# Kernel tuning notes

Hardware: AMD Instinct MI355X
Metric: run time of the kernel (lower is better)

Reference implementation:

```python
import jax, jax.numpy as jnp
import numpy as np

B, N, E, D, H, L = 1024, 64, 1024, 128, 4, 2
C = D // H          # per-head out_channels
K = 5               # options per attribute
LN_EPS = 1e-5


def setup_inputs() -> dict:
    key = jax.random.key(0)
    ks = jax.random.split(key, 22)
    s = 0.05
    inp = {
        'x': jax.random.randint(ks[0], (B, N), 0, K),
        'edge_index': jax.random.randint(ks[1], (2, E), 0, N),
        'edge_attr': jax.random.uniform(ks[2], (E, 1), jnp.float32),
        # tokenizer params
        'attr_emb': jax.random.normal(ks[3], (N, D), jnp.float32) * s,
        'opt_emb': jax.random.normal(ks[4], (N, K, D), jnp.float32) * s,
        'prior': jnp.ones((N, 1), jnp.float32),
        # GATv2 params, stacked over layers
        'Wl': jax.random.normal(ks[5], (L, D, D), jnp.float32) * s,
        'bl': jnp.zeros((L, D), jnp.float32),
        'Wr': jax.random.normal(ks[6], (L, D, D), jnp.float32) * s,
        'br': jnp.zeros((L, D), jnp.float32),
        'We': jax.random.normal(ks[7], (L, 1, D), jnp.float32) * s,
        'att': jax.random.normal(ks[8], (L, H, C), jnp.float32) * s,
        'conv_bias': jnp.zeros((L, D), jnp.float32),
        'ln_g': jnp.ones((L, D), jnp.float32),
        'ln_b': jnp.zeros((L, D), jnp.float32),
        # reliability head
        'W1': jax.random.normal(ks[9], (2 * D, D), jnp.float32) * s,
        'b1': jnp.zeros((D,), jnp.float32),
        'W2': jax.random.normal(ks[10], (D, 1), jnp.float32) * s,
        'b2': jnp.zeros((1,), jnp.float32),
    }
    return inp


def _forward(x, edge_index, edge_attr, attr_emb, opt_emb, prior,
             Wl, bl, Wr, br, We, att, conv_bias, ln_g, ln_b, W1, b1, W2, b2):
    Bb, n = x.shape
    # Tokenizer: token_i = p_i * (E_attr[i] + E_val[i](x_i))
    val = opt_emb[jnp.arange(n)[None, :], x]                 # [B,n,D]
    T0 = (attr_emb[None] + val) * prior[None]                # [B,n,D]

    src, dst = edge_index[0], edge_index[1]
    h = T0
    for l in range(Wl.shape[0]):
        xl = (h @ Wl[l] + bl[l]).reshape(Bb, n, H, C)        # source transform
        xr = (h @ Wr[l] + br[l]).reshape(Bb, n, H, C)        # target transform
        e = (edge_attr @ We[l]).reshape(1, E, H, C)          # edge embedding
        msg = xl[:, src]                                     # [B,E,H,C]
        z = jax.nn.leaky_relu(msg + xr[:, dst] + e, 0.2)
        alpha = jnp.einsum('behc,hc->beh', z, att[l])        # [B,E,H]
        # segment softmax over incoming edges per target node
        mx = jnp.full((Bb, n, H), -jnp.inf, alpha.dtype).at[:, dst].max(alpha)
        ex = jnp.exp(alpha - mx[:, dst])
        den = jnp.zeros((Bb, n, H), alpha.dtype).at[:, dst].add(ex)
        a = ex / den[:, dst]                                 # normalized attention
        out = jnp.zeros((Bb, n, H, C), h.dtype).at[:, dst].add(msg * a[..., None])
        g = out.reshape(Bb, n, D) + conv_bias[l]
        mu = g.mean(-1, keepdims=True)
        var = g.var(-1, keepdims=True)
        g = (g - mu) / jnp.sqrt(var + LN_EPS) * ln_g[l] + ln_b[l]
        g = jax.nn.elu(g)
        h = h + g                                            # residual

    hat_T = jnp.concatenate([T0, h], axis=-1)                # [B,n,2D]
    rel = jax.nn.sigmoid(jax.nn.relu(hat_T @ W1 + b1) @ W2 + b2)[..., 0]  # [B,n]
    rw = rel[..., None]
    f_scale = (h * rw).sum(1) / (rw.sum(1) + 1e-8)           # [B,D]
    return f_scale, rel, hat_T


def reference(x, edge_index, edge_attr, attr_emb, opt_emb, prior,
              Wl, bl, Wr, br, We, att, conv_bias, ln_g, ln_b, W1, b1, W2, b2):
    return _forward(x, edge_index, edge_attr, attr_emb, opt_emb, prior,
                    Wl, bl, Wr, br, We, att, conv_bias, ln_g, ln_b, W1, b1, W2, b2)
```

## Files before the change

kernel.cpp:

```cpp
#include <hip/hip_runtime.h>
#include <hip/hip_bf16.h>

#define Bv 1024
#define Nv 64
#define Ev 1024
#define Dv 128
#define Hv 4
#define Lv 2
#define Kv 5
#define PAD 130

typedef __hip_bfloat16 bf16;
typedef __attribute__((ext_vector_type(8))) short bf16x8_t;
typedef __attribute__((ext_vector_type(4))) float f32x4_t;

__device__ __forceinline__ float b2f(bf16 v) { return __bfloat162float(v); }
__device__ __forceinline__ bf16  f2b(float v) { return __float2bfloat16(v); }

__device__ bf16 g_pWl[(size_t)Lv * 2 * Dv * Dv];
__device__ bf16 g_pWr[(size_t)Lv * 2 * Dv * Dv];
__device__ bf16 g_pW1[(size_t)2 * 2 * Dv * Dv];

__device__ __forceinline__ void unpack2(unsigned int u, float& lo, float& hi) {
    union { unsigned int u; float f; } a, b;
    a.u = u << 16;
    b.u = u & 0xffff0000u;
    lo = a.f; hi = b.f;
}

__device__ __forceinline__ bf16x8_t load_a_frag(const bf16* buf, int elem_idx) {
    const unsigned int* p = (const unsigned int*)buf;
    union { bf16x8_t v; unsigned int u[4]; } r;
    int d = elem_idx >> 1;
    r.u[0] = p[d]; r.u[1] = p[d + 1]; r.u[2] = p[d + 2]; r.u[3] = p[d + 3];
    return r.v;
}

__global__ void build_csr(const int* __restrict__ edge_index,
                          int* __restrict__ off, int* __restrict__ eid)
{
    __shared__ int cnt[Nv];
    int tid = threadIdx.x;
    if (tid < Nv) cnt[tid] = 0;
    __syncthreads();
    for (int e = tid; e < Ev; e += blockDim.x)
        atomicAdd(&cnt[edge_index[Ev + e]], 1);
    __syncthreads();
    if (tid == 0) {
        int s = 0;
        for (int t = 0; t < Nv; ++t) { int c = cnt[t]; off[t] = s; cnt[t] = s; s += c; }
        off[Nv] = s;
    }
    __syncthreads();
    for (int e = tid; e < Ev; e += blockDim.x) {
        int d = edge_index[Ev + e];
        int pos = atomicAdd(&cnt[d], 1);
        eid[pos] = e;
    }
}

__device__ void pack_mat(const float* __restrict__ W, bf16* __restrict__ out,
                         int K, int tid, int nth)
{
    const int total = K * 128;
    for (int e = tid; e < total; e += nth) {
        int f    = e >> 9;
        int rem  = e & 511;
        int lane = rem >> 3;
        int i    = rem & 7;
        int kk   = f >> 3;
        int nt   = f & 7;
        int col  = nt * 16 + (lane & 15);
        int k    = kk * 32 + (lane >> 4) * 8 + i;
        float w  = W[k * 128 + col];
        bf16 hi  = f2b(w);
        out[e]         = hi;
        out[total + e] = f2b(w - b2f(hi));
    }
}

__global__ void pack_weights(const float* __restrict__ Wl, const float* __restrict__ Wr,
                             const float* __restrict__ W1)
{
    const int nth = gridDim.x * blockDim.x;
    const int tid = blockIdx.x * blockDim.x + threadIdx.x;
    for (int l = 0; l < Lv; ++l) {
        pack_mat(Wl + (size_t)l * Dv * Dv, g_pWl + (size_t)l * 2 * Dv * Dv, Dv, tid, nth);
        pack_mat(Wr + (size_t)l * Dv * Dv, g_pWr + (size_t)l * 2 * Dv * Dv, Dv, tid, nth);
    }
    pack_mat(W1, g_pW1, 2 * Dv, tid, nth);
}

__global__ __launch_bounds__(512, 2)
void gat_fused(const int* __restrict__ x, const int* __restrict__ edge_index,
               const float* __restrict__ edge_attr, const float* __restrict__ attr_emb,
               const float* __restrict__ opt_emb, const float* __restrict__ prior,
               const float* __restrict__ bl, const float* __restrict__ br,
               const float* __restrict__ We, const float* __restrict__ att,
               const float* __restrict__ conv_bias, const float* __restrict__ ln_g,
               const float* __restrict__ ln_b,
               const float* __restrict__ b1, const float* __restrict__ W2,
               const float* __restrict__ b2,
               const int* __restrict__ csr_off, const int* __restrict__ csr_eid,
               float* __restrict__ out_fscale, float* __restrict__ out_rel,
               float* __restrict__ out_hatT)
{
    const int b = blockIdx.x;
    const int tid = threadIdx.x;

    __shared__ __align__(16) bf16 hs [Nv * PAD];
    __shared__ __align__(16) bf16 xls[Nv * PAD];
    __shared__ __align__(16) bf16 xrs[Nv * PAD];
    __shared__ bf16 alphas[Ev * Hv];
    __shared__ float red [Nv * 8];
    __shared__ float red2[Nv * 8];
    __shared__ float wecol[Dv];
    __shared__ float attv [Dv];
    __shared__ float relbuf[Nv];

    for (int idx = tid; idx < Nv * Dv; idx += 512) {
        int n = idx >> 7, d = idx & 127;
        float t0 = (attr_emb[n * Dv + d] + opt_emb[(n * Kv + x[b * Nv + n]) * Dv + d])
                   * prior[n];
        hs[n * PAD + d] = f2b(t0);
    }

    for (int l = 0; l < Lv; ++l) {
        if (tid < Dv) {
            wecol[tid] = We[l * Dv + tid];
            attv[tid]  = att[l * Dv + tid];
        }
        __syncthreads();

        {
            const int w = tid >> 6, lane = tid & 63;
            const int row16 = lane & 15, kg = lane >> 4;
            const bf16* pB = (w < 4) ? (g_pWl + (size_t)l * 2 * Dv * Dv)
                                     : (g_pWr + (size_t)l * 2 * Dv * Dv);
            const int wc = (w & 3) * 32;
            f32x4_t acc[4][2];
            #pragma unroll
            for (int mt = 0; mt < 4; ++mt)
                #pragma unroll
                for (int nt = 0; nt < 2; ++nt)
                    acc[mt][nt] = (f32x4_t){0.f, 0.f, 0.f, 0.f};

            #pragma unroll
            for (int kk = 0; kk < 4; ++kk) {
                const int kb = kk * 32 + kg * 8;
                bf16x8_t a[4];
                #pragma unroll
                for (int mt = 0; mt < 4; ++mt)
                    a[mt] = load_a_frag(hs, (mt * 16 + row16) * PAD + kb);
                #pragma unroll
                for (int nt = 0; nt < 2; ++nt) {
                    const int f = kk * 8 + (w & 3) * 2 + nt;
                    bf16x8_t bh  = *(const bf16x8_t*)&pB[(size_t)(f * 64 + lane) * 8];
                    bf16x8_t blo = *(const bf16x8_t*)&pB[Dv * Dv + (size_t)(f * 64 + lane) * 8];
                    #pragma unroll
                    for (int mt = 0; mt < 4; ++mt) {
                        acc[mt][nt] = __builtin_amdgcn_mfma_f32_16x16x32_bf16(
                                          a[mt], bh, acc[mt][nt], 0, 0, 0);
                        acc[mt][nt] = __builtin_amdgcn_mfma_f32_16x16x32_bf16(
                                          a[mt], blo, acc[mt][nt], 0, 0, 0);
                    }
                }
            }
            bf16* dst = (w < 4) ? xls : xrs;
            const float* bias = (w < 4) ? (bl + l * Dv) : (br + l * Dv);
            #pragma unroll
            for (int mt = 0; mt < 4; ++mt)
                #pragma unroll
                for (int nt = 0; nt < 2; ++nt) {
                    const int col = wc + nt * 16 + row16;
                    #pragma unroll
                    for (int r = 0; r < 4; ++r) {
                        const int row = mt * 16 + kg * 4 + r;
                        dst[row * PAD + col] = f2b(acc[mt][nt][r] + bias[col]);
                    }
                }
        }
        __syncthreads();

        {
            const int h = (tid >> 6) & 3, half = tid >> 8, lane = tid & 63;
            for (int it = 0; it < 8; ++it) {
                int e = (half * 8 + it) * 64 + lane;
                int s = edge_index[e], t = edge_index[Ev + e];
                float ea = edge_attr[e];
                float acc = 0.f;
                int bs = s * PAD + h * 32, bt = t * PAD + h * 32;
                #pragma unroll
                for (int c = 0; c < 32; c += 2) {
                    float xl0, xl1, xr0, xr1;
                    unpack2(*(const unsigned int*)&xls[bs + c], xl0, xl1);
                    unpack2(*(const unsigned int*)&xrs[bt + c], xr0, xr1);
                    float z0 = xl0 + xr0 + ea * wecol[h * 32 + c];
                    float z1 = xl1 + xr1 + ea * wecol[h * 32 + c + 1];
                    z0 = z0 > 0.f ? z0 : 0.2f * z0;
                    z1 = z1 > 0.f ? z1 : 0.2f * z1;
                    acc += z0 * attv[h * 32 + c] + z1 * attv[h * 32 + c + 1];
                }
                alphas[e * Hv + h] = f2b(acc);
            }
        }
        __syncthreads();

        {
            const int t = tid & 63, h = (tid >> 6) & 3, half = tid >> 8;
            const int ch0 = h * 32 + half * 16;
            int beg = csr_off[t], end = csr_off[t + 1];
            float mx = -3e38f;
            for (int idx = beg; idx < end; ++idx)
                mx = fmaxf(mx, b2f(alphas[csr_eid[idx] * Hv + h]));
            float acc[16];
            #pragma unroll
            for (int c = 0; c < 16; ++c) acc[c] = 0.f;
            float den = 0.f;
            for (int idx = beg; idx < end; ++idx) {
                int e = csr_eid[idx];
                int s = edge_index[e];
                float ex = expf(b2f(alphas[e * Hv + h]) - mx);
                den += ex;
                int bs = s * PAD + ch0;
                #pragma unroll
                for (int c = 0; c < 16; c += 2) {
                    float m0, m1;
                    unpack2(*(const unsigned int*)&xls[bs + c], m0, m1);
                    acc[c] += ex * m0; acc[c + 1] += ex * m1;
                }
            }
            float inv_den = (end > beg) ? 1.f / den : 0.f;
            float sum = 0.f, sumsq = 0.f;
            #pragma unroll
            for (int c = 0; c < 16; ++c) {
                float g = acc[c] * inv_den + conv_bias[l * Dv + ch0 + c];
                acc[c] = g;
                sum += g; sumsq += g * g;
            }
            red [t * 8 + h * 2 + half] = sum;
            red2[t * 8 + h * 2 + half] = sumsq;
            __syncthreads();
            float mu = 0.f, ms = 0.f;
            #pragma unroll
            for (int j = 0; j < 8; ++j) { mu += red[t * 8 + j]; ms += red2[t * 8 + j]; }
            mu *= (1.f / 128.f); ms *= (1.f / 128.f);
            float rstd = rsqrtf(ms - mu * mu + 1e-5f);
            #pragma unroll
            for (int c = 0; c < 16; ++c) {
                float g = (acc[c] - mu) * rstd * ln_g[l * Dv + ch0 + c]
                          + ln_b[l * Dv + ch0 + c];
                g = g > 0.f ? g : (expf(g) - 1.f);
                int hi = t * PAD + ch0 + c;
                hs[hi] = f2b(b2f(hs[hi]) + g);
            }
        }
        __syncthreads();
    }

    if (tid < Dv) wecol[tid] = W2[tid];
    for (int idx = tid; idx < Nv * Dv; idx += 512) {
        int n = idx >> 7, d = idx & 127;
        float t0 = (attr_emb[n * Dv + d] + opt_emb[(n * Kv + x[b * Nv + n]) * Dv + d])
                   * prior[n];
        xrs[n * PAD + d] = f2b(t0);
        size_t rb = ((size_t)(b * Nv + n)) * (2 * Dv);
        out_hatT[rb + d]      = t0;
        out_hatT[rb + Dv + d] = b2f(hs[n * PAD + d]);
    }
    __syncthreads();

    {
        const int w = tid >> 6, lane = tid & 63;
        const int row16 = lane & 15, kg = lane >> 4;
        f32x4_t acc[4];
        #pragma unroll
        for (int mt = 0; mt < 4; ++mt)
            acc[mt] = (f32x4_t){0.f, 0.f, 0.f, 0.f};

        #pragma unroll
        for (int kk = 0; kk < 8; ++kk) {
            const bf16* asrc = (kk < 4) ? xrs : hs;
            const int kb = (kk & 3) * 32 + kg * 8;
            bf16x8_t a[4];
            #pragma unroll
            for (int mt = 0; mt < 4; ++mt)
                a[mt] = load_a_frag(asrc, (mt * 16 + row16) * PAD + kb);
            const int f = kk * 8 + w;
            bf16x8_t bh  = *(const bf16x8_t*)&g_pW1[(size_t)(f * 64 + lane) * 8];
            bf16x8_t blo = *(const bf16x8_t*)&g_pW1[(size_t)2 * Dv * Dv + (size_t)(f * 64 + lane) * 8];
            #pragma unroll
            for (int mt = 0; mt < 4; ++mt) {
                acc[mt] = __builtin_amdgcn_mfma_f32_16x16x32_bf16(a[mt], bh,  acc[mt], 0, 0, 0);
                acc[mt] = __builtin_amdgcn_mfma_f32_16x16x32_bf16(a[mt], blo, acc[mt], 0, 0, 0);
            }
        }
        #pragma unroll
        for (int mt = 0; mt < 4; ++mt) {
            const int col = w * 16 + row16;
            #pragma unroll
            for (int r = 0; r < 4; ++r) {
                const int row = mt * 16 + kg * 4 + r;
                float v = acc[mt][r] + b1[col];
                xls[row * PAD + col] = f2b(v > 0.f ? v : 0.f);
            }
        }
    }
    __syncthreads();

    {
        const int t = tid & 63, h = (tid >> 6) & 3, half = tid >> 8;
        const int ch0 = h * 32 + half * 16;
        float s = 0.f;
        #pragma unroll
        for (int c = 0; c < 16; c += 2) {
            float h0, h1;
            unpack2(*(const unsigned int*)&xls[t * PAD + ch0 + c], h0, h1);
            s += h0 * wecol[ch0 + c] + h1 * wecol[ch0 + c + 1];
        }
        red[t * 8 + h * 2 + half] = s;
        __syncthreads();
        if (h == 0 && half == 0) {
            float z = b2[0];
            #pragma unroll
            for (int j = 0; j < 8; ++j) z += red[t * 8 + j];
            float r = 1.f / (1.f + expf(-z));
            relbuf[t] = r;
            out_rel[b * Nv + t] = r;
        }
    }
    __syncthreads();

    if (tid < Dv) {
        float num = 0.f, den = 0.f;
        for (int n = 0; n < Nv; ++n) {
            float r = relbuf[n];
            num += b2f(hs[n * PAD + tid]) * r;
            den += r;
        }
        out_fscale[b * Dv + tid] = num / (den + 1e-8f);
    }
}

extern "C" void kernel_launch(void* const* d_in, const int* in_sizes, int n_in,
                              void* d_out, int out_size, void* d_ws, size_t ws_size,
                              hipStream_t stream)
{
    const int*   x          = (const int*)  d_in[0];
    const int*   edge_index = (const int*)  d_in[1];
    const float* edge_attr  = (const float*)d_in[2];
    const float* attr_emb   = (const float*)d_in[3];
    const float* opt_emb    = (const float*)d_in[4];
    const float* prior      = (const float*)d_in[5];
    const float* Wl         = (const float*)d_in[6];
    const float* bl         = (const float*)d_in[7];
    const float* Wr         = (const float*)d_in[8];
    const float* br         = (const float*)d_in[9];
    const float* We         = (const float*)d_in[10];
    const float* att        = (const float*)d_in[11];
    const float* conv_bias  = (const float*)d_in[12];
    const float* ln_g       = (const float*)d_in[13];
    const float* ln_b       = (const float*)d_in[14];
    const float* W1         = (const float*)d_in[15];
    const float* b1         = (const float*)d_in[16];
    const float* W2         = (const float*)d_in[17];
    const float* b2         = (const float*)d_in[18];

    int* csr_off = (int*)d_ws;
    int* csr_eid = (int*)d_ws + 128;

    float* out        = (float*)d_out;
    float* out_fscale = out;
    float* out_rel    = out + (size_t)Bv * Dv;
    float* out_hatT   = out + (size_t)Bv * Dv + (size_t)Bv * Nv;

    build_csr<<<1, 256, 0, stream>>>(edge_index, csr_off, csr_eid);
    pack_weights<<<64, 256, 0, stream>>>(Wl, Wr, W1);
    gat_fused<<<Bv, 512, 0, stream>>>(x, edge_index, edge_attr, attr_emb, opt_emb,
                                      prior, bl, br, We, att, conv_bias,
                                      ln_g, ln_b, b1, W2, b2,
                                      csr_off, csr_eid,
                                      out_fscale, out_rel, out_hatT);
}
```

Measured before the change: 309.6 us.

## Rewrite LeakyReLU attention as linear terms plus ReLU, pack f32x2 math, merge prep kernels

Uses the identity leaky(z) = 0.2*z + 0.8*relu(z) so the linear part of the attention score factors into per-node dot products (att·xl, att·xr), computed once per node, plus a per-head constant for the edge term. The per-edge loop keeps only a max with zero and packed two-wide FMAs. The aggregation, LayerNorm and reliability-head loops are rewritten with f32x2 vector types to encourage packed FP32 instructions. The CSR build and weight-packing kernels are merged into one launch, which also precomputes the edge constant. This adds an extra reduction pass and barrier per layer and changes rounding, since the per-node dot products come from bf16 values.

```diff
diff --git a/kernel.cpp b/kernel.cpp
--- a/kernel.cpp
+++ b/kernel.cpp
@@ -13,6 +13,7 @@
 typedef __hip_bfloat16 bf16;
 typedef __attribute__((ext_vector_type(8))) short bf16x8_t;
 typedef __attribute__((ext_vector_type(4))) float f32x4_t;
+typedef __attribute__((ext_vector_type(2))) float f32x2_t;
 
 __device__ __forceinline__ float b2f(bf16 v) { return __bfloat162float(v); }
 __device__ __forceinline__ bf16  f2b(float v) { return __float2bfloat16(v); }
@@ -20,12 +21,26 @@
 __device__ bf16 g_pWl[(size_t)Lv * 2 * Dv * Dv];
 __device__ bf16 g_pWr[(size_t)Lv * 2 * Dv * Dv];
 __device__ bf16 g_pW1[(size_t)2 * 2 * Dv * Dv];
+__device__ float g_K[Lv * Hv];
 
 __device__ __forceinline__ void unpack2(unsigned int u, float& lo, float& hi) {
     union { unsigned int u; float f; } a, b;
     a.u = u << 16;
     b.u = u & 0xffff0000u;
     lo = a.f; hi = b.f;
+}
+
+__device__ __forceinline__ f32x2_t unpack2v(unsigned int u) {
+    union { unsigned int u; float f; } a, b;
+    a.u = u << 16;
+    b.u = u & 0xffff0000u;
+    return (f32x2_t){a.f, b.f};
+}
+
+__device__ __forceinline__ unsigned int pack2v(f32x2_t v) {
+    union { bf16 b; unsigned short u; } lo, hi;
+    lo.b = f2b(v.x); hi.b = f2b(v.y);
+    return (unsigned int)lo.u | ((unsigned int)hi.u << 16);
 }
 
 __device__ __forceinline__ bf16x8_t load_a_frag(const bf16* buf, int elem_idx) {
@@ -34,29 +49,6 @@
     int d = elem_idx >> 1;
     r.u[0] = p[d]; r.u[1] = p[d + 1]; r.u[2] = p[d + 2]; r.u[3] = p[d + 3];
     return r.v;
-}
-
-__global__ void build_csr(const int* __restrict__ edge_index,
-                          int* __restrict__ off, int* __restrict__ eid)
-{
-    __shared__ int cnt[Nv];
-    int tid = threadIdx.x;
-    if (tid < Nv) cnt[tid] = 0;
-    __syncthreads();
-    for (int e = tid; e < Ev; e += blockDim.x)
-        atomicAdd(&cnt[edge_index[Ev + e]], 1);
-    __syncthreads();
-    if (tid == 0) {
-        int s = 0;
-        for (int t = 0; t < Nv; ++t) { int c = cnt[t]; off[t] = s; cnt[t] = s; s += c; }
-        off[Nv] = s;
-    }
-    __syncthreads();
-    for (int e = tid; e < Ev; e += blockDim.x) {
-        int d = edge_index[Ev + e];
-        int pos = atomicAdd(&cnt[d], 1);
-        eid[pos] = e;
-    }
 }
 
 __device__ void pack_mat(const float* __restrict__ W, bf16* __restrict__ out,
@@ -79,16 +71,48 @@
     }
 }
 
-__global__ void pack_weights(const float* __restrict__ Wl, const float* __restrict__ Wr,
-                             const float* __restrict__ W1)
+__global__ void prep(const int* __restrict__ edge_index,
+                     int* __restrict__ off, int* __restrict__ eid,
+                     const float* __restrict__ Wl, const float* __restrict__ Wr,
+                     const float* __restrict__ W1, const float* __restrict__ We,
+                     const float* __restrict__ att)
 {
-    const int nth = gridDim.x * blockDim.x;
-    const int tid = blockIdx.x * blockDim.x + threadIdx.x;
+    const int bid = blockIdx.x;
+    if (bid == 0) {
+        __shared__ int cnt[Nv];
+        int tid = threadIdx.x;
+        if (tid < Nv) cnt[tid] = 0;
+        __syncthreads();
+        for (int e = tid; e < Ev; e += blockDim.x)
+            atomicAdd(&cnt[edge_index[Ev + e]], 1);
+        __syncthreads();
+        if (tid == 0) {
+            int s = 0;
+            for (int t = 0; t < Nv; ++t) { int c = cnt[t]; off[t] = s; cnt[t] = s; s += c; }
+            off[Nv] = s;
+        }
+        __syncthreads();
+        for (int e = tid; e < Ev; e += blockDim.x) {
+            int d = edge_index[Ev + e];
+            int pos = atomicAdd(&cnt[d], 1);
+            eid[pos] = e;
+        }
+        return;
+    }
+    const int nth = 64 * 256;
+    const int tid = (bid - 1) * 256 + threadIdx.x;
     for (int l = 0; l < Lv; ++l) {
         pack_mat(Wl + (size_t)l * Dv * Dv, g_pWl + (size_t)l * 2 * Dv * Dv, Dv, tid, nth);
         pack_mat(Wr + (size_t)l * Dv * Dv, g_pWr + (size_t)l * 2 * Dv * Dv, Dv, tid, nth);
     }
     pack_mat(W1, g_pW1, 2 * Dv, tid, nth);
+    if (bid == 1 && threadIdx.x < Lv * Hv) {
+        int l = threadIdx.x / Hv, h = threadIdx.x % Hv;
+        float k = 0.f;
+        for (int c = 0; c < 32; ++c)
+            k += att[l * Dv + h * 32 + c] * We[l * Dv + h * 32 + c];
+        g_K[threadIdx.x] = 0.2f * k;
+    }
 }
 
 __global__ __launch_bounds__(512, 2)
@@ -96,11 +120,11 @@
                const float* __restrict__ edge_attr, const float* __restrict__ attr_emb,
                const float* __restrict__ opt_emb, const float* __restrict__ prior,
                const float* __restrict__ bl, const float* __restrict__ br,
-               const float* __restrict__ We, const float* __restrict__ att,
                const float* __restrict__ conv_bias, const float* __restrict__ ln_g,
                const float* __restrict__ ln_b,
                const float* __restrict__ b1, const float* __restrict__ W2,
                const float* __restrict__ b2,
+               const float* __restrict__ We, const float* __restrict__ att,
                const int* __restrict__ csr_off, const int* __restrict__ csr_eid,
                float* __restrict__ out_fscale, float* __restrict__ out_rel,
                float* __restrict__ out_hatT)
@@ -112,10 +136,10 @@
     __shared__ __align__(16) bf16 xls[Nv * PAD];
     __shared__ __align__(16) bf16 xrs[Nv * PAD];
     __shared__ bf16 alphas[Ev * Hv];
-    __shared__ float red [Nv * 8];
-    __shared__ float red2[Nv * 8];
-    __shared__ float wecol[Dv];
-    __shared__ float attv [Dv];
+    __shared__ __align__(16) float red [Nv * 8];
+    __shared__ __align__(16) float red2[Nv * 8];
+    __shared__ __align__(16) float wecol[Dv];
+    __shared__ __align__(16) float attv [Dv];
     __shared__ float relbuf[Nv];
 
     for (int idx = tid; idx < Nv * Dv; idx += 512) {
@@ -183,25 +207,44 @@
         __syncthreads();
 
         {
+            const int t = tid & 63, h = (tid >> 6) & 3, half = tid >> 8;
+            const int ch0 = h * 32 + half * 16;
+            f32x2_t dl2 = {0.f, 0.f}, dr2 = {0.f, 0.f};
+            #pragma unroll
+            for (int c = 0; c < 16; c += 2) {
+                f32x2_t a2 = *(const f32x2_t*)&attv[ch0 + c];
+                dl2 += a2 * unpack2v(*(const unsigned int*)&xls[t * PAD + ch0 + c]);
+                dr2 += a2 * unpack2v(*(const unsigned int*)&xrs[t * PAD + ch0 + c]);
+            }
+            red [t * 8 + h * 2 + half] = dl2.x + dl2.y;
+            red2[t * 8 + h * 2 + half] = dr2.x + dr2.y;
+        }
+        __syncthreads();
+
+        {
             const int h = (tid >> 6) & 3, half = tid >> 8, lane = tid & 63;
+            const float k02 = g_K[l * Hv + h];
+            const f32x2_t zero2 = {0.f, 0.f};
             for (int it = 0; it < 8; ++it) {
                 int e = (half * 8 + it) * 64 + lane;
                 int s = edge_index[e], t = edge_index[Ev + e];
                 float ea = edge_attr[e];
-                float acc = 0.f;
+                f32x2_t ea2 = {ea, ea};
+                f32x2_t acc2 = {0.f, 0.f};
                 int bs = s * PAD + h * 32, bt = t * PAD + h * 32;
                 #pragma unroll
                 for (int c = 0; c < 32; c += 2) {
-                    float xl0, xl1, xr0, xr1;
-                    unpack2(*(const unsigned int*)&xls[bs + c], xl0, xl1);
-                    unpack2(*(const unsigned int*)&xrs[bt + c], xr0, xr1);
-                    float z0 = xl0 + xr0 + ea * wecol[h * 32 + c];
-                    float z1 = xl1 + xr1 + ea * wecol[h * 32 + c + 1];
-                    z0 = z0 > 0.f ? z0 : 0.2f * z0;
-                    z1 = z1 > 0.f ? z1 : 0.2f * z1;
-                    acc += z0 * attv[h * 32 + c] + z1 * attv[h * 32 + c + 1];
+                    f32x2_t xl2 = unpack2v(*(const unsigned int*)&xls[bs + c]);
+                    f32x2_t xr2 = unpack2v(*(const unsigned int*)&xrs[bt + c]);
+                    f32x2_t we2 = *(const f32x2_t*)&wecol[h * 32 + c];
+                    f32x2_t at2 = *(const f32x2_t*)&attv [h * 32 + c];
+                    f32x2_t v   = xl2 + xr2 + ea2 * we2;
+                    acc2 += at2 * __builtin_elementwise_max(v, zero2);
                 }
-                alphas[e * Hv + h] = f2b(acc);
+                float dL = red [s * 8 + h * 2] + red [s * 8 + h * 2 + 1];
+                float dR = red2[t * 8 + h * 2] + red2[t * 8 + h * 2 + 1];
+                float alpha = 0.2f * (dL + dR) + k02 * ea + 0.8f * (acc2.x + acc2.y);
+                alphas[e * Hv + h] = f2b(alpha);
             }
         }
         __syncthreads();
@@ -213,46 +256,50 @@
             float mx = -3e38f;
             for (int idx = beg; idx < end; ++idx)
                 mx = fmaxf(mx, b2f(alphas[csr_eid[idx] * Hv + h]));
-            float acc[16];
-            #pragma unroll
-            for (int c = 0; c < 16; ++c) acc[c] = 0.f;
+            f32x2_t acc2[8];
+            #pragma unroll
+            for (int j = 0; j < 8; ++j) acc2[j] = (f32x2_t){0.f, 0.f};
             float den = 0.f;
             for (int idx = beg; idx < end; ++idx) {
                 int e = csr_eid[idx];
                 int s = edge_index[e];
                 float ex = expf(b2f(alphas[e * Hv + h]) - mx);
                 den += ex;
+                f32x2_t ex2 = {ex, ex};
                 int bs = s * PAD + ch0;
                 #pragma unroll
-                for (int c = 0; c < 16; c += 2) {
-                    float m0, m1;
-                    unpack2(*(const unsigned int*)&xls[bs + c], m0, m1);
-                    acc[c] += ex * m0; acc[c + 1] += ex * m1;
-                }
+                for (int j = 0; j < 8; ++j)
+                    acc2[j] += ex2 * unpack2v(*(const unsigned int*)&xls[bs + 2 * j]);
             }
             float inv_den = (end > beg) ? 1.f / den : 0.f;
-            float sum = 0.f, sumsq = 0.f;
-            #pragma unroll
-            for (int c = 0; c < 16; ++c) {
-                float g = acc[c] * inv_den + conv_bias[l * Dv + ch0 + c];
-                acc[c] = g;
-                sum += g; sumsq += g * g;
-            }
-            red [t * 8 + h * 2 + half] = sum;
-            red2[t * 8 + h * 2 + half] = sumsq;
+            f32x2_t id2 = {inv_den, inv_den};
+            f32x2_t sum2 = {0.f, 0.f}, sq2 = {0.f, 0.f};
+            #pragma unroll
+            for (int j = 0; j < 8; ++j) {
+                f32x2_t cb = *(const f32x2_t*)&conv_bias[l * Dv + ch0 + 2 * j];
+                f32x2_t g  = acc2[j] * id2 + cb;
+                acc2[j] = g;
+                sum2 += g; sq2 += g * g;
+            }
+            red [t * 8 + h * 2 + half] = sum2.x + sum2.y;
+            red2[t * 8 + h * 2 + half] = sq2.x + sq2.y;
             __syncthreads();
             float mu = 0.f, ms = 0.f;
             #pragma unroll
             for (int j = 0; j < 8; ++j) { mu += red[t * 8 + j]; ms += red2[t * 8 + j]; }
             mu *= (1.f / 128.f); ms *= (1.f / 128.f);
             float rstd = rsqrtf(ms - mu * mu + 1e-5f);
-            #pragma unroll
-            for (int c = 0; c < 16; ++c) {
-                float g = (acc[c] - mu) * rstd * ln_g[l * Dv + ch0 + c]
-                          + ln_b[l * Dv + ch0 + c];
-                g = g > 0.f ? g : (expf(g) - 1.f);
-                int hi = t * PAD + ch0 + c;
-                hs[hi] = f2b(b2f(hs[hi]) + g);
+            f32x2_t mu2 = {mu, mu}, rs2 = {rstd, rstd};
+            #pragma unroll
+            for (int j = 0; j < 8; ++j) {
+                f32x2_t lg = *(const f32x2_t*)&ln_g[l * Dv + ch0 + 2 * j];
+                f32x2_t lb = *(const f32x2_t*)&ln_b[l * Dv + ch0 + 2 * j];
+                f32x2_t g  = (acc2[j] - mu2) * rs2 * lg + lb;
+                g.x = g.x > 0.f ? g.x : (expf(g.x) - 1.f);
+                g.y = g.y > 0.f ? g.y : (expf(g.y) - 1.f);
+                unsigned int* hp = (unsigned int*)&hs[t * PAD + ch0 + 2 * j];
+                f32x2_t hv = unpack2v(*hp) + g;
+                *hp = pack2v(hv);
             }
         }
         __syncthreads();
@@ -311,14 +358,13 @@
     {
         const int t = tid & 63, h = (tid >> 6) & 3, half = tid >> 8;
         const int ch0 = h * 32 + half * 16;
-        float s = 0.f;
+        f32x2_t s2 = {0.f, 0.f};
         #pragma unroll
         for (int c = 0; c < 16; c += 2) {
-            float h0, h1;
-            unpack2(*(const unsigned int*)&xls[t * PAD + ch0 + c], h0, h1);
-            s += h0 * wecol[ch0 + c] + h1 * wecol[ch0 + c + 1];
-        }
-        red[t * 8 + h * 2 + half] = s;
+            f32x2_t h2 = unpack2v(*(const unsigned int*)&xls[t * PAD + ch0 + c]);
+            s2 += h2 * *(const f32x2_t*)&wecol[ch0 + c];
+        }
+        red[t * 8 + h * 2 + half] = s2.x + s2.y;
         __syncthreads();
         if (h == 0 && half == 0) {
             float z = b2[0];
@@ -374,11 +420,10 @@
     float* out_rel    = out + (size_t)Bv * Dv;
     float* out_hatT   = out + (size_t)Bv * Dv + (size_t)Bv * Nv;
 
-    build_csr<<<1, 256, 0, stream>>>(edge_index, csr_off, csr_eid);
-    pack_weights<<<64, 256, 0, stream>>>(Wl, Wr, W1);
+    prep<<<65, 256, 0, stream>>>(edge_index, csr_off, csr_eid, Wl, Wr, W1, We, att);
     gat_fused<<<Bv, 512, 0, stream>>>(x, edge_index, edge_attr, attr_emb, opt_emb,
-                                      prior, bl, br, We, att, conv_bias,
-                                      ln_g, ln_b, b1, W2, b2,
+                                      prior, bl, br, conv_bias,
+                                      ln_g, ln_b, b1, W2, b2, We, att,
                                       csr_off, csr_eid,
                                       out_fscale, out_rel, out_hatT);
 }
```

Result: faster. 302.7 us (-2.2%).
